# Kernel optimization log

Hardware: AMD Instinct MI355X
Metric: run time of the kernel (lower is better)

The kernel has to match this reference:

```python
import jax, jax.numpy as jnp
import numpy as np

B, IN, OUT, ZD = 128, 1024, 1024, 128


def setup_inputs() -> dict:
    key = jax.random.key(0)
    ks = jax.random.split(key, 6)
    x = jax.random.normal(ks[0], (B, IN), dtype=jnp.float32)
    z = jax.random.normal(ks[1], (B, ZD), dtype=jnp.float32)
    base_weight = jax.random.normal(ks[2], (OUT, IN), dtype=jnp.float32) * (2.0 / IN) ** 0.5
    # delta_weight_head: nn.Linear(z_dim, out*in)
    lim_w = 1.0 / np.sqrt(ZD)
    dw_W = jax.random.uniform(ks[3], (OUT * IN, ZD), dtype=jnp.float32, minval=-lim_w, maxval=lim_w)
    dw_b = jnp.zeros((OUT * IN,), dtype=jnp.float32)
    base_bias = jnp.zeros((OUT,), dtype=jnp.float32)
    # delta_bias_head: nn.Linear(z_dim, out)
    db_W = jax.random.uniform(ks[4], (OUT, ZD), dtype=jnp.float32, minval=-lim_w, maxval=lim_w)
    db_b = jnp.zeros((OUT,), dtype=jnp.float32)
    return {"x": x, "z": z, "base_weight": base_weight, "dw_W": dw_W,
            "dw_b": dw_b, "base_bias": base_bias, "db_W": db_W, "db_b": db_b}


def reference(x, z, base_weight, dw_W, dw_b, base_bias, db_W, db_b):
    Bn = x.shape[0]
    # per-sample delta weight: [B, out*in] -> [B, out, in]
    delta_w = (z @ dw_W.T + dw_b).reshape(Bn, OUT, IN)
    w = base_weight[None, :, :] + delta_w
    out = jnp.einsum('boi,bi->bo', w, x)  # batched GEMV
    delta_b = z @ db_W.T + db_b
    out = out + base_bias + delta_b
    return out
```

## Files before the change

kernel.cpp:

```cpp
#include <hip/hip_runtime.h>
#include <hip/hip_bf16.h>
#include <stdint.h>


#define IN_N  1024
#define OUT_N 1024
#define ZD_N  128
#define KK    (IN_N * ZD_N)
#define KSPLIT 64
#define KSPAN  (KK / KSPLIT)
#define BK     64
#define NCHUNK (KSPAN / BK)

typedef __attribute__((ext_vector_type(8))) short s16x8;
typedef __attribute__((ext_vector_type(4))) float f32x4;

union BF8 { s16x8 v; short4 h[2]; __hip_bfloat162 b[4]; };

__global__ __launch_bounds__(256) void init_small(
    const float* __restrict__ x, const float* __restrict__ z,
    const float* __restrict__ bw, const float* __restrict__ dwb,
    const float* __restrict__ bbias, const float* __restrict__ dbW,
    const float* __restrict__ dbb, float* __restrict__ out)
{
    const int tid = threadIdx.x;
    const int b   = tid & 127;
    const int oh  = tid >> 7;
    const int o0  = blockIdx.x * 4 + oh * 2;

    float acc0 = bbias[o0]     + dbb[o0];
    float acc1 = bbias[o0 + 1] + dbb[o0 + 1];

    const float* zrow = z + (size_t)b * ZD_N;
    for (int k = 0; k < ZD_N; k += 4) {
        float4 zv = *(const float4*)(zrow + k);
        float4 d0 = *(const float4*)(dbW + (size_t)o0 * ZD_N + k);
        float4 d1 = *(const float4*)(dbW + (size_t)(o0 + 1) * ZD_N + k);
        acc0 += zv.x * d0.x + zv.y * d0.y + zv.z * d0.z + zv.w * d0.w;
        acc1 += zv.x * d1.x + zv.y * d1.y + zv.z * d1.z + zv.w * d1.w;
    }
    const float* xrow = x + (size_t)b * IN_N;
    for (int i = 0; i < IN_N; i += 4) {
        float4 xv = *(const float4*)(xrow + i);
        float4 w0 = *(const float4*)(bw  + (size_t)o0 * IN_N + i);
        float4 v0 = *(const float4*)(dwb + (size_t)o0 * IN_N + i);
        float4 w1 = *(const float4*)(bw  + (size_t)(o0 + 1) * IN_N + i);
        float4 v1 = *(const float4*)(dwb + (size_t)(o0 + 1) * IN_N + i);
        acc0 += xv.x * (w0.x + v0.x) + xv.y * (w0.y + v0.y)
              + xv.z * (w0.z + v0.z) + xv.w * (w0.w + v0.w);
        acc1 += xv.x * (w1.x + v1.x) + xv.y * (w1.y + v1.y)
              + xv.z * (w1.z + v1.z) + xv.w * (w1.w + v1.w);
    }
    out[(size_t)b * OUT_N + o0]     = acc0;
    out[(size_t)b * OUT_N + o0 + 1] = acc1;
}

__global__ __launch_bounds__(256, 2) void hyper_gemm(
    const float* __restrict__ x,
    const float* __restrict__ z,
    const float* __restrict__ dwW,
    float* __restrict__ out)
{
    __shared__ s16x8 blds[2][8 * 128];

    const int tid  = threadIdx.x;
    const int lane = tid & 63;
    const int w    = tid >> 6;
    const int wm   = (w & 1) * 64;
    const int wn   = (w >> 1) * 64;
    const int q    = lane >> 4;
    const int l16  = lane & 15;

    const int nb = blockIdx.x & 7;
    const int ks = blockIdx.x >> 3;
    const int n0 = nb * 128;
    const long long kk0 = (long long)ks * KSPAN;

    f32x4 acc[4][4];
#pragma unroll
    for (int mt = 0; mt < 4; ++mt)
#pragma unroll
        for (int nt = 0; nt < 4; ++nt) acc[mt][nt] = (f32x4)0.0f;

    const int q4   = tid & 15;
    const int nrow = tid >> 4;
    const int gst  = q4 >> 1;
    const int hst  = q4 & 1;

    float4 breg[8];
#define LOAD_B(c)                                                                   \
    {                                                                               \
        _Pragma("unroll") for (int j = 0; j < 8; ++j) {                             \
            int n = j * 16 + nrow;                                                  \
            breg[j] = *(const float4*)(dwW + (size_t)(n0 + n) * KK +                \
                                       (size_t)(kk0 + (c) * BK + q4 * 4));          \
        }                                                                           \
    }

    LOAD_B(0);

    for (int c = 0; c < NCHUNK; ++c) {
#pragma unroll
        for (int j = 0; j < 8; ++j) {
            int n = j * 16 + nrow;
            union { short4 s; __hip_bfloat162 b[2]; } u;
            u.b[0] = __float22bfloat162_rn(make_float2(breg[j].x, breg[j].y));
            u.b[1] = __float22bfloat162_rn(make_float2(breg[j].z, breg[j].w));
            ((short4*)&blds[c & 1][gst * 128 + (n ^ gst)])[hst] = u.s;
        }
        __syncthreads();
        if (c + 1 < NCHUNK) LOAD_B(c + 1);

        const long long kkb = kk0 + (long long)c * BK;
        const int i_c = (int)(kkb >> 7);
        const int kzb = (int)(kkb & 127);
        const s16x8* bufp = &blds[c & 1][0];

#pragma unroll
        for (int s = 0; s < 2; ++s) {
            const int gq = s * 4 + q;
            s16x8 bfr[4];
#pragma unroll
            for (int nt = 0; nt < 4; ++nt) {
                int nl = wn + nt * 16 + l16;
                bfr[nt] = bufp[gq * 128 + (nl ^ gq)];
            }
#pragma unroll
            for (int mt = 0; mt < 4; ++mt) {
                const int m = wm + mt * 16 + l16;
                const float xv = x[(size_t)m * IN_N + i_c];
                const float* zp = z + (size_t)m * ZD_N + kzb + s * 32 + q * 8;
                float4 z0 = *(const float4*)(zp);
                float4 z1 = *(const float4*)(zp + 4);
                BF8 af;
                af.b[0] = __float22bfloat162_rn(make_float2(xv * z0.x, xv * z0.y));
                af.b[1] = __float22bfloat162_rn(make_float2(xv * z0.z, xv * z0.w));
                af.b[2] = __float22bfloat162_rn(make_float2(xv * z1.x, xv * z1.y));
                af.b[3] = __float22bfloat162_rn(make_float2(xv * z1.z, xv * z1.w));
#pragma unroll
                for (int nt = 0; nt < 4; ++nt)
                    acc[mt][nt] = __builtin_amdgcn_mfma_f32_16x16x32_bf16(
                        af.v, bfr[nt], acc[mt][nt], 0, 0, 0);
            }
        }
        __syncthreads();
    }

#pragma unroll
    for (int mt = 0; mt < 4; ++mt) {
        const int mbase = wm + mt * 16 + q * 4;
#pragma unroll
        for (int nt = 0; nt < 4; ++nt) {
            const int o = n0 + wn + nt * 16 + l16;
#pragma unroll
            for (int r = 0; r < 4; ++r)
                atomicAdd(&out[(size_t)(mbase + r) * OUT_N + o], acc[mt][nt][r]);
        }
    }
#undef LOAD_B
}

extern "C" void kernel_launch(void* const* d_in, const int* in_sizes, int n_in,
                              void* d_out, int out_size, void* d_ws, size_t ws_size,
                              hipStream_t stream) {
    const float* x     = (const float*)d_in[0];
    const float* z     = (const float*)d_in[1];
    const float* bw    = (const float*)d_in[2];
    const float* dwW   = (const float*)d_in[3];
    const float* dwb   = (const float*)d_in[4];
    const float* bbias = (const float*)d_in[5];
    const float* dbW   = (const float*)d_in[6];
    const float* dbb   = (const float*)d_in[7];
    float* out = (float*)d_out;

    hipLaunchKernelGGL(init_small, dim3(256), dim3(256), 0, stream,
                       x, z, bw, dwb, bbias, dbW, dbb, out);
    hipLaunchKernelGGL(hyper_gemm, dim3(512), dim3(256), 0, stream, x, z, dwW, out);
}
```

Before: 876.6 us.

## Load B fragments directly to registers, drop LDS, replace atomics with workspace reduction

The GEMM kernel stops staging the dwW tile through double-buffered LDS. Each lane now loads its own B fragment straight from global memory into registers and converts it to bf16, which removes the __syncthreads barriers. Split-K partial results go to a workspace buffer and a separate reduce kernel sums them, replacing float atomics on the output. init_small now gives one output per thread over twice as many blocks. The direct loads are strided per lane, so they may coalesce worse than the old cooperative loads. The workspace adds 32 MB of writes and reads plus an extra launch.

New measurement: 1.031 ms. +17.6%, slower.

```diff
diff --git a/kernel.cpp b/kernel.cpp
--- a/kernel.cpp
+++ b/kernel.cpp
@@ -9,13 +9,11 @@
 #define KK    (IN_N * ZD_N)
 #define KSPLIT 64
 #define KSPAN  (KK / KSPLIT)
-#define BK     64
-#define NCHUNK (KSPAN / BK)
 
 typedef __attribute__((ext_vector_type(8))) short s16x8;
 typedef __attribute__((ext_vector_type(4))) float f32x4;
 
-union BF8 { s16x8 v; short4 h[2]; __hip_bfloat162 b[4]; };
+union BF8 { s16x8 v; __hip_bfloat162 b[4]; };
 
 __global__ __launch_bounds__(256) void init_small(
     const float* __restrict__ x, const float* __restrict__ z,
@@ -25,44 +23,36 @@
 {
     const int tid = threadIdx.x;
     const int b   = tid & 127;
-    const int oh  = tid >> 7;
-    const int o0  = blockIdx.x * 4 + oh * 2;
+    const int o   = blockIdx.x * 2 + (tid >> 7);
 
-    float acc0 = bbias[o0]     + dbb[o0];
-    float acc1 = bbias[o0 + 1] + dbb[o0 + 1];
+    float acc = bbias[o] + dbb[o];
 
     const float* zrow = z + (size_t)b * ZD_N;
+    const float* dr   = dbW + (size_t)o * ZD_N;
     for (int k = 0; k < ZD_N; k += 4) {
         float4 zv = *(const float4*)(zrow + k);
-        float4 d0 = *(const float4*)(dbW + (size_t)o0 * ZD_N + k);
-        float4 d1 = *(const float4*)(dbW + (size_t)(o0 + 1) * ZD_N + k);
-        acc0 += zv.x * d0.x + zv.y * d0.y + zv.z * d0.z + zv.w * d0.w;
-        acc1 += zv.x * d1.x + zv.y * d1.y + zv.z * d1.z + zv.w * d1.w;
+        float4 dv = *(const float4*)(dr + k);
+        acc += zv.x * dv.x + zv.y * dv.y + zv.z * dv.z + zv.w * dv.w;
     }
-    const float* xrow = x + (size_t)b * IN_N;
+    const float* xrow = x  + (size_t)b * IN_N;
+    const float* wr   = bw + (size_t)o * IN_N;
+    const float* vr   = dwb + (size_t)o * IN_N;
     for (int i = 0; i < IN_N; i += 4) {
         float4 xv = *(const float4*)(xrow + i);
-        float4 w0 = *(const float4*)(bw  + (size_t)o0 * IN_N + i);
-        float4 v0 = *(const float4*)(dwb + (size_t)o0 * IN_N + i);
-        float4 w1 = *(const float4*)(bw  + (size_t)(o0 + 1) * IN_N + i);
-        float4 v1 = *(const float4*)(dwb + (size_t)(o0 + 1) * IN_N + i);
-        acc0 += xv.x * (w0.x + v0.x) + xv.y * (w0.y + v0.y)
-              + xv.z * (w0.z + v0.z) + xv.w * (w0.w + v0.w);
-        acc1 += xv.x * (w1.x + v1.x) + xv.y * (w1.y + v1.y)
-              + xv.z * (w1.z + v1.z) + xv.w * (w1.w + v1.w);
+        float4 wv = *(const float4*)(wr + i);
+        float4 vv = *(const float4*)(vr + i);
+        acc += xv.x * (wv.x + vv.x) + xv.y * (wv.y + vv.y)
+             + xv.z * (wv.z + vv.z) + xv.w * (wv.w + vv.w);
     }
-    out[(size_t)b * OUT_N + o0]     = acc0;
-    out[(size_t)b * OUT_N + o0 + 1] = acc1;
+    out[(size_t)b * OUT_N + o] = acc;
 }
 
 __global__ __launch_bounds__(256, 2) void hyper_gemm(
     const float* __restrict__ x,
     const float* __restrict__ z,
     const float* __restrict__ dwW,
-    float* __restrict__ out)
+    float* __restrict__ ws)
 {
-    __shared__ s16x8 blds[2][8 * 128];
-
     const int tid  = threadIdx.x;
     const int lane = tid & 63;
     const int w    = tid >> 6;
@@ -82,82 +72,82 @@
 #pragma unroll
         for (int nt = 0; nt < 4; ++nt) acc[mt][nt] = (f32x4)0.0f;
 
-    const int q4   = tid & 15;
-    const int nrow = tid >> 4;
-    const int gst  = q4 >> 1;
-    const int hst  = q4 & 1;
+    const float* brow[4];
+    const float* zrow[4];
+    const float* xrowp[4];
+#pragma unroll
+    for (int nt = 0; nt < 4; ++nt)
+        brow[nt] = dwW + (size_t)(n0 + wn + nt * 16 + l16) * KK + kk0 + q * 8;
+#pragma unroll
+    for (int mt = 0; mt < 4; ++mt) {
+        const int m = wm + mt * 16 + l16;
+        zrow[mt]  = z + (size_t)m * ZD_N + q * 8;
+        xrowp[mt] = x + (size_t)m * IN_N;
+    }
+    const int i0 = (int)(kk0 >> 7);
 
-    float4 breg[8];
-#define LOAD_B(c)                                                                   \
-    {                                                                               \
-        _Pragma("unroll") for (int j = 0; j < 8; ++j) {                             \
-            int n = j * 16 + nrow;                                                  \
-            breg[j] = *(const float4*)(dwW + (size_t)(n0 + n) * KK +                \
-                                       (size_t)(kk0 + (c) * BK + q4 * 4));          \
-        }                                                                           \
-    }
+#pragma unroll 1
+    for (int e = 0; e < KSPAN / 128; ++e) {
+        float xv[4];
+#pragma unroll
+        for (int mt = 0; mt < 4; ++mt) xv[mt] = xrowp[mt][i0 + e];
 
-    LOAD_B(0);
-
-    for (int c = 0; c < NCHUNK; ++c) {
-#pragma unroll
-        for (int j = 0; j < 8; ++j) {
-            int n = j * 16 + nrow;
-            union { short4 s; __hip_bfloat162 b[2]; } u;
-            u.b[0] = __float22bfloat162_rn(make_float2(breg[j].x, breg[j].y));
-            u.b[1] = __float22bfloat162_rn(make_float2(breg[j].z, breg[j].w));
-            ((short4*)&blds[c & 1][gst * 128 + (n ^ gst)])[hst] = u.s;
-        }
-        __syncthreads();
-        if (c + 1 < NCHUNK) LOAD_B(c + 1);
-
-        const long long kkb = kk0 + (long long)c * BK;
-        const int i_c = (int)(kkb >> 7);
-        const int kzb = (int)(kkb & 127);
-        const s16x8* bufp = &blds[c & 1][0];
-
-#pragma unroll
-        for (int s = 0; s < 2; ++s) {
-            const int gq = s * 4 + q;
+#pragma unroll 1
+        for (int s = 0; s < 4; ++s) {
+            const int off = e * 128 + s * 32;
             s16x8 bfr[4];
 #pragma unroll
             for (int nt = 0; nt < 4; ++nt) {
-                int nl = wn + nt * 16 + l16;
-                bfr[nt] = bufp[gq * 128 + (nl ^ gq)];
+                float4 b0 = *(const float4*)(brow[nt] + off);
+                float4 b1 = *(const float4*)(brow[nt] + off + 4);
+                BF8 u;
+                u.b[0] = __float22bfloat162_rn(make_float2(b0.x, b0.y));
+                u.b[1] = __float22bfloat162_rn(make_float2(b0.z, b0.w));
+                u.b[2] = __float22bfloat162_rn(make_float2(b1.x, b1.y));
+                u.b[3] = __float22bfloat162_rn(make_float2(b1.z, b1.w));
+                bfr[nt] = u.v;
             }
 #pragma unroll
             for (int mt = 0; mt < 4; ++mt) {
-                const int m = wm + mt * 16 + l16;
-                const float xv = x[(size_t)m * IN_N + i_c];
-                const float* zp = z + (size_t)m * ZD_N + kzb + s * 32 + q * 8;
+                const float* zp = zrow[mt] + s * 32;
                 float4 z0 = *(const float4*)(zp);
                 float4 z1 = *(const float4*)(zp + 4);
                 BF8 af;
-                af.b[0] = __float22bfloat162_rn(make_float2(xv * z0.x, xv * z0.y));
-                af.b[1] = __float22bfloat162_rn(make_float2(xv * z0.z, xv * z0.w));
-                af.b[2] = __float22bfloat162_rn(make_float2(xv * z1.x, xv * z1.y));
-                af.b[3] = __float22bfloat162_rn(make_float2(xv * z1.z, xv * z1.w));
+                af.b[0] = __float22bfloat162_rn(make_float2(xv[mt] * z0.x, xv[mt] * z0.y));
+                af.b[1] = __float22bfloat162_rn(make_float2(xv[mt] * z0.z, xv[mt] * z0.w));
+                af.b[2] = __float22bfloat162_rn(make_float2(xv[mt] * z1.x, xv[mt] * z1.y));
+                af.b[3] = __float22bfloat162_rn(make_float2(xv[mt] * z1.z, xv[mt] * z1.w));
 #pragma unroll
                 for (int nt = 0; nt < 4; ++nt)
                     acc[mt][nt] = __builtin_amdgcn_mfma_f32_16x16x32_bf16(
                         af.v, bfr[nt], acc[mt][nt], 0, 0, 0);
             }
         }
-        __syncthreads();
     }
 
+    float* wsb = ws + (size_t)ks * (128 * 1024) + n0;
 #pragma unroll
     for (int mt = 0; mt < 4; ++mt) {
         const int mbase = wm + mt * 16 + q * 4;
 #pragma unroll
         for (int nt = 0; nt < 4; ++nt) {
-            const int o = n0 + wn + nt * 16 + l16;
+            const int n = wn + nt * 16 + l16;
 #pragma unroll
             for (int r = 0; r < 4; ++r)
-                atomicAdd(&out[(size_t)(mbase + r) * OUT_N + o], acc[mt][nt][r]);
+                wsb[(size_t)(mbase + r) * 1024 + n] = acc[mt][nt][r];
         }
     }
-#undef LOAD_B
+}
+
+__global__ __launch_bounds__(256) void reduce_out(const float* __restrict__ ws,
+                                                  float* __restrict__ out)
+{
+    const int idx = blockIdx.x * 256 + threadIdx.x;
+    float s = out[idx];
+#pragma unroll
+    for (int k = 0; k < KSPLIT; ++k)
+        s += ws[(size_t)k * (128 * 1024) + idx];
+    out[idx] = s;
 }
 
 extern "C" void kernel_launch(void* const* d_in, const int* in_sizes, int n_in,
@@ -172,8 +162,10 @@
     const float* dbW   = (const float*)d_in[6];
     const float* dbb   = (const float*)d_in[7];
     float* out = (float*)d_out;
+    float* ws  = (float*)d_ws;
 
-    hipLaunchKernelGGL(init_small, dim3(256), dim3(256), 0, stream,
+    hipLaunchKernelGGL(init_small, dim3(512), dim3(256), 0, stream,
                        x, z, bw, dwb, bbias, dbW, dbb, out);
-    hipLaunchKernelGGL(hyper_gemm, dim3(512), dim3(256), 0, stream, x, z, dwW, out);
+    hipLaunchKernelGGL(hyper_gemm, dim3(512), dim3(256), 0, stream, x, z, dwW, ws);
+    hipLaunchKernelGGL(reduce_out, dim3(512), dim3(256), 0, stream, ws, out);
 }
```
